# Optimization experiments

Hardware: AMD Instinct MI355X
Metric: run time of the kernel (lower is better)

Reference implementation:

```python
import jax, jax.numpy as jnp
import numpy as np
from jax import lax

# Module defaults: set_params never called, so t_min=0, t_max=1 (from __init__),
# and multiplier/kernel_mul take the identity value 1.0. noise = 0.0.
T_MIN = 0.0
T_MAX = 1.0
KERNEL_MUL = 1.0
MULTIPLIER = 1.0
PAD = 3  # 'same' padding for 7x7 kernel: (kh-1)//2


def setup_inputs() -> dict:
    key = jax.random.key(0)
    k1, k2, k3, k4 = jax.random.split(key, 4)
    # spiking times lie in [t_min, t_max] = [0, 1]
    tj = jax.random.uniform(k1, (8, 1, 256, 256), dtype=jnp.float32)
    kernel = jax.random.normal(k2, (384, 1, 7, 7), dtype=jnp.float32) * 0.1
    B = jax.random.normal(k3, (384, 1), dtype=jnp.float32) * 0.01
    D_i = jax.random.normal(k4, (9, 384), dtype=jnp.float32) * 0.01
    return {"tj": tj, "kernel": kernel, "B": B, "D_i": D_i}


def reference(tj, kernel, B, D_i):
    # Original: pad tj with value t_min, unfold into patches, append a constant
    # column one_as_time = t_min - 1, append row B.T/multiplier to W, then
    # ti = (tj - t_min) @ W + (t_max - t_min - D_i[0]) + t_min, clamped to t_max.
    # Equivalent fused form: conv2d on (tj - t_min) with zero padding (pad value
    # t_min cancels after the subtraction); the appended bias column contributes
    # (t_min - 1 - t_min) * B / multiplier = -B / multiplier per output channel.
    x = tj - T_MIN  # [B, 1, H, W]
    conv = lax.conv_general_dilated(
        x,
        kernel * KERNEL_MUL,  # [F, 1, 7, 7]
        window_strides=(1, 1),
        padding=[(PAD, PAD), (PAD, PAD)],
        dimension_numbers=("NCHW", "OIHW", "NCHW"),
    )  # [B, F, H, W]
    threshold = T_MAX - T_MIN - D_i[0]          # [F]
    bias = -B[:, 0] / MULTIPLIER                # [F]
    ti = conv + (bias + threshold + T_MIN)[None, :, None, None]
    # torch.where(ti < t_max, ti, t_max) == elementwise min with t_max
    return jnp.minimum(ti, T_MAX)
```

## Files before the change

kernel.cpp:

```cpp
#include <hip/hip_runtime.h>
#include <stdint.h>
#include <stddef.h>

typedef __attribute__((ext_vector_type(8))) short short8;
typedef __attribute__((ext_vector_type(4))) float f32x4;

#define NB 8
#define NC 384
#define HH 256
#define WW 256
#define PR 264
#define PROWS 264
#define PLANE (PR * PROWS)
#define IMG_ELEMS (NB * PLANE)
#define IMG_BLOCKS 2178
#define NFRAG 3072
#define EXTRA_BLOCKS 14
#define PREP_BLOCKS (IMG_BLOCKS + EXTRA_BLOCKS)

#define GRID 4096
#define ITERS 8

__device__ __forceinline__ unsigned short f2bf(float f) {
    unsigned int u = __float_as_uint(f);
    return (unsigned short)((u + 0x7FFFu + ((u >> 16) & 1u)) >> 16);
}

__global__ __launch_bounds__(256) void prep_kernel(
    const float* __restrict__ tj, const float* __restrict__ kern,
    const float* __restrict__ Bv, const float* __restrict__ Di,
    unsigned short* __restrict__ tjp, unsigned short* __restrict__ wfrag,
    float* __restrict__ bias)
{
    int bid = blockIdx.x, tid = threadIdx.x;
    if (bid < IMG_BLOCKS) {
        int idx = bid * 256 + tid;
        int b = idx / PLANE;
        int rem = idx - b * PLANE;
        int r = rem / PR;
        int c = rem - r * PR;
        int hh = r - 3, ww = c - 3;
        float v = 0.f;
        if (hh >= 0 && hh < HH && ww >= 0 && ww < WW)
            v = tj[(b * HH + hh) * WW + ww];
        tjp[idx] = f2bf(v);
    } else {
        int idx = (bid - IMG_BLOCKS) * 256 + tid;
        if (idx < NFRAG) {
            int lane = idx & 63;
            int fk = idx >> 6;
            int kc = fk & 1, ct = fk >> 1;
            int ch = ct * 16 + (lane & 15);
            int kh = kc * 4 + (lane >> 4);
            unsigned int tmp[8];
            #pragma unroll
            for (int j = 0; j < 8; ++j) {
                float v = 0.f;
                if (kh < 7 && j < 7) v = kern[(ch * 7 + kh) * 7 + j];
                tmp[j] = f2bf(v);
            }
            uint4 pk;
            pk.x = tmp[0] | (tmp[1] << 16);
            pk.y = tmp[2] | (tmp[3] << 16);
            pk.z = tmp[4] | (tmp[5] << 16);
            pk.w = tmp[6] | (tmp[7] << 16);
            ((uint4*)wfrag)[idx] = pk;
        } else if (idx < NFRAG + NC) {
            int c = idx - NFRAG;
            bias[c] = 1.0f - Di[c] - Bv[c];
        }
    }
}

__global__ __launch_bounds__(512, 6) void conv_main(
    const unsigned short* __restrict__ tjp,
    const unsigned short* __restrict__ wfrag,
    const float* __restrict__ bias,
    float* __restrict__ out)
{
    int tid = threadIdx.x;
    int wave = tid >> 6, lane = tid & 63;
    int q = lane >> 4, n = lane & 15;
    int ct0 = wave * 3;

    short8 wf[6];
    const short8* wp = (const short8*)wfrag;
    #pragma unroll
    for (int i = 0; i < 6; ++i)
        wf[i] = wp[(ct0 * 2 + i) * 64 + lane];

    float bv[12];
    #pragma unroll
    for (int t = 0; t < 12; ++t) {
        int ct = t >> 2, reg = t & 3;
        bv[t] = bias[(ct0 + ct) * 16 + q * 4 + reg];
    }

    for (int t = 0; t < ITERS; ++t) {
        int i = blockIdx.x * ITERS + t;
        int wt = i & 15;
        int h  = (i >> 4) & 255;
        int b  = i >> 12;
        int w0 = wt * 16;

        const unsigned short* src = tjp + b * PLANE + (h + q) * PR + w0 + n;
        short8 pb0, pb1;
        __builtin_memcpy(&pb0, src, 16);
        __builtin_memcpy(&pb1, src + 4 * PR, 16);

        unsigned int base0 = ((unsigned int)(b * NC + ct0 * 16 + q * 4) << 16)
                           + ((unsigned int)h << 8) + (unsigned int)(w0 + n);
        #pragma unroll
        for (int ct = 0; ct < 3; ++ct) {
            f32x4 acc = {0.f, 0.f, 0.f, 0.f};
            acc = __builtin_amdgcn_mfma_f32_16x16x32_bf16(wf[ct * 2 + 0], pb0, acc, 0, 0, 0);
            acc = __builtin_amdgcn_mfma_f32_16x16x32_bf16(wf[ct * 2 + 1], pb1, acc, 0, 0, 0);
            unsigned int base = base0 + ((unsigned int)ct << 20);
            #pragma unroll
            for (int reg = 0; reg < 4; ++reg) {
                float v = acc[reg] + bv[ct * 4 + reg];
                v = fminf(v, 1.0f);
                out[base + ((unsigned int)reg << 16)] = v;
            }
        }
    }
}

extern "C" void kernel_launch(void* const* d_in, const int* in_sizes, int n_in,
                              void* d_out, int out_size, void* d_ws, size_t ws_size,
                              hipStream_t stream) {
    (void)in_sizes; (void)n_in; (void)out_size; (void)ws_size;
    const float* tj   = (const float*)d_in[0];
    const float* kern = (const float*)d_in[1];
    const float* Bv   = (const float*)d_in[2];
    const float* Di   = (const float*)d_in[3];
    float* out = (float*)d_out;

    unsigned short* tjp   = (unsigned short*)d_ws;
    unsigned short* wfrag = (unsigned short*)((char*)d_ws + (size_t)IMG_ELEMS * 2);
    float* bias           = (float*)((char*)d_ws + (size_t)IMG_ELEMS * 2 + NFRAG * 16);

    prep_kernel<<<PREP_BLOCKS, 256, 0, stream>>>(tj, kern, Bv, Di, tjp, wfrag, bias);
    conv_main<<<GRID, 512, 0, stream>>>(tjp, wfrag, bias, out);
}
```

Measured before the change: 909.8 us.

## Transpose MFMA operands for vectorized output stores and add shifted image copy

Swaps the MFMA operand roles so each lane's accumulator holds four consecutive output columns of one channel, which allows 16-byte vector stores instead of scattered scalar stores. A second bf16 padded image, shifted by one element, is written so odd-column lanes can issue 4-byte-aligned 16-byte loads. Work is remapped so each block handles one channel tile, one batch and a 16-row strip, with each wave covering 32 columns. This costs an extra padded image write in the prep kernel and adds workspace use.

Result: faster. 833.3 us (-8.4%).

```diff
diff --git a/kernel.cpp b/kernel.cpp
--- a/kernel.cpp
+++ b/kernel.cpp
@@ -4,6 +4,9 @@
 
 typedef __attribute__((ext_vector_type(8))) short short8;
 typedef __attribute__((ext_vector_type(4))) float f32x4;
+typedef __attribute__((ext_vector_type(4))) unsigned int uint4v;
+
+struct __attribute__((packed, aligned(4))) u4a4 { uint4v v; };
 
 #define NB 8
 #define NC 384
@@ -18,32 +21,42 @@
 #define EXTRA_BLOCKS 14
 #define PREP_BLOCKS (IMG_BLOCKS + EXTRA_BLOCKS)
 
-#define GRID 4096
-#define ITERS 8
+#define GRID 3072
+#define HITERS 16
 
 __device__ __forceinline__ unsigned short f2bf(float f) {
     unsigned int u = __float_as_uint(f);
     return (unsigned short)((u + 0x7FFFu + ((u >> 16) & 1u)) >> 16);
 }
 
+__device__ __forceinline__ float padval(const float* __restrict__ tj, int idx) {
+    int b = idx / PLANE;
+    int rem = idx - b * PLANE;
+    int r = rem / PR;
+    int c = rem - r * PR;
+    int hh = r - 3, ww = c - 3;
+    if (b < NB && hh >= 0 && hh < HH && ww >= 0 && ww < WW)
+        return tj[(b * HH + hh) * WW + ww];
+    return 0.f;
+}
+
+__device__ __forceinline__ short8 ld16a4(const void* p) {
+    union { uint4v u; short8 s; } cv;
+    cv.u = ((const u4a4*)p)->v;
+    return cv.s;
+}
+
 __global__ __launch_bounds__(256) void prep_kernel(
     const float* __restrict__ tj, const float* __restrict__ kern,
     const float* __restrict__ Bv, const float* __restrict__ Di,
-    unsigned short* __restrict__ tjp, unsigned short* __restrict__ wfrag,
-    float* __restrict__ bias)
+    unsigned short* __restrict__ tjp_e, unsigned short* __restrict__ tjp_o,
+    unsigned short* __restrict__ wfrag, float* __restrict__ bias)
 {
     int bid = blockIdx.x, tid = threadIdx.x;
     if (bid < IMG_BLOCKS) {
         int idx = bid * 256 + tid;
-        int b = idx / PLANE;
-        int rem = idx - b * PLANE;
-        int r = rem / PR;
-        int c = rem - r * PR;
-        int hh = r - 3, ww = c - 3;
-        float v = 0.f;
-        if (hh >= 0 && hh < HH && ww >= 0 && ww < WW)
-            v = tj[(b * HH + hh) * WW + ww];
-        tjp[idx] = f2bf(v);
+        tjp_e[idx] = f2bf(padval(tj, idx));
+        tjp_o[idx] = f2bf((idx + 1 < IMG_ELEMS) ? padval(tj, idx + 1) : 0.f);
     } else {
         int idx = (bid - IMG_BLOCKS) * 256 + tid;
         if (idx < NFRAG) {
@@ -73,7 +86,8 @@
 }
 
 __global__ __launch_bounds__(512, 6) void conv_main(
-    const unsigned short* __restrict__ tjp,
+    const unsigned short* __restrict__ tjp_e,
+    const unsigned short* __restrict__ tjp_o,
     const unsigned short* __restrict__ wfrag,
     const float* __restrict__ bias,
     float* __restrict__ out)
@@ -81,48 +95,49 @@
     int tid = threadIdx.x;
     int wave = tid >> 6, lane = tid & 63;
     int q = lane >> 4, n = lane & 15;
-    int ct0 = wave * 3;
 
-    short8 wf[6];
+    int bid = blockIdx.x;
+    int b  = bid / 384;
+    int r1 = bid - b * 384;
+    int ct = r1 >> 4;
+    int hc = r1 & 15;
+
     const short8* wp = (const short8*)wfrag;
-    #pragma unroll
-    for (int i = 0; i < 6; ++i)
-        wf[i] = wp[(ct0 * 2 + i) * 64 + lane];
+    short8 wf0 = wp[(ct * 2 + 0) * 64 + lane];
+    short8 wf1 = wp[(ct * 2 + 1) * 64 + lane];
+    float bv = bias[ct * 16 + n];
 
-    float bv[12];
-    #pragma unroll
-    for (int t = 0; t < 12; ++t) {
-        int ct = t >> 2, reg = t & 3;
-        bv[t] = bias[(ct0 + ct) * 16 + q * 4 + reg];
-    }
+    const char* base = (n & 1) ? ((const char*)tjp_o - 2) : (const char*)tjp_e;
 
-    for (int t = 0; t < ITERS; ++t) {
-        int i = blockIdx.x * ITERS + t;
-        int wt = i & 15;
-        int h  = (i >> 4) & 255;
-        int b  = i >> 12;
-        int w0 = wt * 16;
+    int w0 = wave * 32;
+    unsigned int obase = ((unsigned int)(b * NC + ct * 16 + n) << 16) + (unsigned int)(w0 + 4 * q);
 
-        const unsigned short* src = tjp + b * PLANE + (h + q) * PR + w0 + n;
-        short8 pb0, pb1;
-        __builtin_memcpy(&pb0, src, 16);
-        __builtin_memcpy(&pb1, src + 4 * PR, 16);
+    for (int t = 0; t < HITERS; ++t) {
+        int h = hc * HITERS + t;
+        unsigned int e = (unsigned int)(b * PLANE + (h + q) * PR + w0 + n);
+        const char* p = base + 2u * e;
 
-        unsigned int base0 = ((unsigned int)(b * NC + ct0 * 16 + q * 4) << 16)
-                           + ((unsigned int)h << 8) + (unsigned int)(w0 + n);
+        short8 a00 = ld16a4(p);
+        short8 a01 = ld16a4(p + 8 * PR);
+        short8 a10 = ld16a4(p + 32);
+        short8 a11 = ld16a4(p + 32 + 8 * PR);
+
+        f32x4 acc0 = {0.f, 0.f, 0.f, 0.f};
+        f32x4 acc1 = {0.f, 0.f, 0.f, 0.f};
+        acc0 = __builtin_amdgcn_mfma_f32_16x16x32_bf16(a00, wf0, acc0, 0, 0, 0);
+        acc0 = __builtin_amdgcn_mfma_f32_16x16x32_bf16(a01, wf1, acc0, 0, 0, 0);
+        acc1 = __builtin_amdgcn_mfma_f32_16x16x32_bf16(a10, wf0, acc1, 0, 0, 0);
+        acc1 = __builtin_amdgcn_mfma_f32_16x16x32_bf16(a11, wf1, acc1, 0, 0, 0);
+
+        f32x4 r0, r1v;
         #pragma unroll
-        for (int ct = 0; ct < 3; ++ct) {
-            f32x4 acc = {0.f, 0.f, 0.f, 0.f};
-            acc = __builtin_amdgcn_mfma_f32_16x16x32_bf16(wf[ct * 2 + 0], pb0, acc, 0, 0, 0);
-            acc = __builtin_amdgcn_mfma_f32_16x16x32_bf16(wf[ct * 2 + 1], pb1, acc, 0, 0, 0);
-            unsigned int base = base0 + ((unsigned int)ct << 20);
-            #pragma unroll
-            for (int reg = 0; reg < 4; ++reg) {
-                float v = acc[reg] + bv[ct * 4 + reg];
-                v = fminf(v, 1.0f);
-                out[base + ((unsigned int)reg << 16)] = v;
-            }
+        for (int reg = 0; reg < 4; ++reg) {
+            r0[reg]  = fminf(acc0[reg] + bv, 1.0f);
+            r1v[reg] = fminf(acc1[reg] + bv, 1.0f);
         }
+        unsigned int o = obase + ((unsigned int)h << 8);
+        *(f32x4*)(out + o)      = r0;
+        *(f32x4*)(out + o + 16) = r1v;
     }
 }
 
@@ -136,10 +151,12 @@
     const float* Di   = (const float*)d_in[3];
     float* out = (float*)d_out;
 
-    unsigned short* tjp   = (unsigned short*)d_ws;
-    unsigned short* wfrag = (unsigned short*)((char*)d_ws + (size_t)IMG_ELEMS * 2);
-    float* bias           = (float*)((char*)d_ws + (size_t)IMG_ELEMS * 2 + NFRAG * 16);
+    char* ws = (char*)d_ws;
+    unsigned short* tjp_e = (unsigned short*)ws;
+    unsigned short* tjp_o = (unsigned short*)(ws + (size_t)IMG_ELEMS * 2);
+    unsigned short* wfrag = (unsigned short*)(ws + (size_t)IMG_ELEMS * 4);
+    float* bias           = (float*)(ws + (size_t)IMG_ELEMS * 4 + NFRAG * 16);
 
-    prep_kernel<<<PREP_BLOCKS, 256, 0, stream>>>(tj, kern, Bv, Di, tjp, wfrag, bias);
-    conv_main<<<GRID, 512, 0, stream>>>(tjp, wfrag, bias, out);
+    prep_kernel<<<PREP_BLOCKS, 256, 0, stream>>>(tj, kern, Bv, Di, tjp_e, tjp_o, wfrag, bias);
+    conv_main<<<GRID, 512, 0, stream>>>(tjp_e, tjp_o, wfrag, bias, out);
 }
```
